# Kernel optimization log

Hardware: AMD Instinct MI355X
Metric: run time of the kernel (lower is better)

The kernel has to match this reference:

```python
import jax, jax.numpy as jnp
import numpy as np

L = 6      # num_coupling_layers
H = 256    # hidden_dims
B = 131072 # batch
D = 2      # sample_dims (fixed by masks)


def setup_inputs() -> dict:
    key = jax.random.key(0)
    ks = jax.random.split(key, 21)
    x = jax.random.uniform(ks[0], (B, D), jnp.float32, 1e-3, 1.0 - 1e-3)
    def w(k, shape):
        return jax.random.normal(k, shape, jnp.float32) * 0.05
    inp = {"x": x}
    shapes = {"W1": (L, D, H), "B1": (L, H), "W2": (L, H, H), "B2": (L, H),
              "W3": (L, H, H), "B3": (L, H), "W4": (L, H, H), "B4": (L, H),
              "W5": (L, H, D), "B5": (L, D)}
    i = 1
    for pref in ("s", "t"):
        for name, shp in shapes.items():
            inp[pref + name] = w(ks[i], shp)
            i += 1
    return inp


def _net(h, i, W1, B1, W2, B2, W3, B3, W4, B4, W5, B5, final_tanh):
    a = jax.nn.relu(h @ W1[i] + B1[i])
    a = jax.nn.relu(a @ W2[i] + B2[i])
    a = jax.nn.relu(a @ W3[i] + B3[i])
    a = jax.nn.relu(a @ W4[i] + B4[i])
    o = a @ W5[i] + B5[i]
    return jnp.tanh(o) if final_tanh else o


def reference(x, sW1, sB1, sW2, sB2, sW3, sB3, sW4, sB4, sW5, sB5,
              tW1, tB1, tW2, tB2, tW3, tB3, tW4, tB4, tW5, tB5):
    # masks alternate [0,1],[1,0]
    masks = jnp.asarray([[0.0, 1.0], [1.0, 0.0]] * (L // 2), jnp.float32)
    # logit transform
    x = -jnp.log(1.0 / x - 1.0)
    log_det_inv = jnp.zeros(x.shape[0], x.dtype)
    # training=True default -> direction = -1, gate = -1, reversed layer order
    for i in range(L - 1, -1, -1):
        m = masks[i]
        rm = 1.0 - m
        x_masked = x * m
        s = _net(x_masked, i, sW1, sB1, sW2, sB2, sW3, sB3, sW4, sB4, sW5, sB5, True) * rm
        t = _net(x_masked, i, tW1, tB1, tW2, tB2, tW3, tB3, tW4, tB4, tW5, tB5, False) * rm
        # rm*(x*exp(-s) - t*exp(-s)) + x_masked
        x = rm * ((x - t) * jnp.exp(-s)) + x_masked
        log_det_inv = log_det_inv - jnp.sum(s, axis=1)
    x = jax.nn.sigmoid(x)
    return x, log_det_inv
```

## Files before the change

kernel.cpp:

```cpp
#include <hip/hip_runtime.h>
#include <hip/hip_bf16.h>

#define LNUM 6
#define BATCH 131072

typedef __bf16 bf16x8 __attribute__((ext_vector_type(8)));
typedef float f32x16 __attribute__((ext_vector_type(16)));
typedef float f32x4  __attribute__((ext_vector_type(4)));

#define WFRAG_BYTES 131072ul
#define W1B1_OFF 4718592ul
#define BIAS_OFF 4743168ul
#define W5_OFF   4780032ul
#define NPT   2048
#define ZMIN  (-28.f)
#define ZH    (56.f / 2047.f)
#define ZINVH (2047.f / 56.f)
#define TABS_OFF 4793088ul
#define TABT_OFF 4842240ul
#define WS_NEEDED 4891392ul

struct PtrPack { const float* p[21]; };

__global__ void prep_all(PtrPack P, unsigned char* __restrict__ ws) {
    if (blockIdx.x < 288) {
#pragma unroll
        for (int r = 0; r < 4; ++r) {
            int t = blockIdx.x * 1024 + r * 256 + threadIdx.x;
            int blk = t >> 13;
            int e8  = t & 8191;
            int nh  = e8 >> 12;
            int kk  = (e8 >> 8) & 15;
            int nti = (e8 >> 6) & 3;
            int l   = e8 & 63;
            int nt = nh * 4 + nti;
            int n  = nt * 32 + (l & 31);
            int k0 = kk * 16 + (l >> 5) * 8;
            int net = blk / 18, rem = blk % 18;
            int i = rem / 3, g = rem % 3;
            const float* src = P.p[3 + g * 2 + net * 10] + i * 65536;
            bf16x8 v;
#pragma unroll
            for (int jj = 0; jj < 8; ++jj) v[jj] = (__bf16)src[(k0 + jj) * 256 + n];
            *(bf16x8*)(ws + (unsigned long)blk * WFRAG_BYTES + (unsigned)e8 * 16) = v;
        }
        return;
    }
#pragma unroll
    for (int r = 0; r < 8; ++r) {
        int t = (blockIdx.x - 288) * 2048 + r * 256 + threadIdx.x;
        if (t < 6144) {
            int idx = t >> 9, e = t & 511;
            int net = idx / 6, i = idx % 6;
            int j = (i & 1) ? 0 : 1;
            float v;
            if (e < 256) v = P.p[1 + net * 10][i * 512 + j * 256 + e];
            else         v = P.p[2 + net * 10][i * 256 + (e - 256)];
            ((float*)(ws + W1B1_OFF))[t] = v;
        } else if (t < 6144 + 9216) {
            int u = t - 6144;
            int idx = u >> 8, e = u & 255;
            int net = idx / 18, rem = idx % 18, i = rem / 3, g = rem % 3;
            ((float*)(ws + BIAS_OFF))[u] = P.p[4 + g * 2 + net * 10][i * 256 + e];
        } else if (t < 6144 + 9216 + 12 * 272) {
            int u = t - 6144 - 9216;
            int idx = u / 272, e = u % 272;
            int net = idx / 6, i = idx % 6;
            int ud = (i & 1) ? 1 : 0;
            float v = 0.f;
            if (e < 256)      v = P.p[9 + net * 10][i * 512 + e * 2 + ud];
            else if (e == 256) v = P.p[10 + net * 10][i * 2 + ud];
            ((float*)(ws + W5_OFF))[idx * 272 + e] = v;
        }
    }
}

#define L_A   0
#define L_ZG  65536
#define L_RED 66048
#define L_TOT 70144

__device__ __forceinline__ unsigned pk2(float a, float b) {
    unsigned short ua = __builtin_bit_cast(unsigned short, (__bf16)a);
    unsigned short ub = __builtin_bit_cast(unsigned short, (__bf16)b);
    return (unsigned)ua | ((unsigned)ub << 16);
}

__global__ __launch_bounds__(512, 1) void tab_eval(
        const unsigned char* __restrict__ ws, float* __restrict__ tabS,
        float* __restrict__ tabT) {
    __shared__ __align__(16) unsigned char lds[L_TOT];
    const int tid = threadIdx.x;
    const int wv = tid >> 6, lane = tid & 63;
    const int li = lane & 31, hi = lane >> 5;
    const int nn = blockIdx.x >> 4;
    const int tile = blockIdx.x & 15;
    float* zG  = (float*)(lds + L_ZG);
    float* red = (float*)(lds + L_RED);
    const float* w1b1_g = (const float*)(ws + W1B1_OFF);
    const float* bias_g = (const float*)(ws + BIAS_OFF);
    const float* w5_g   = (const float*)(ws + W5_OFF);

    const unsigned char* aaBase = lds + L_A + (unsigned)lane * 16;
    unsigned char* const stBase = lds + L_A + (unsigned)(li * 16 + hi * 8);

    if (tid < 128) zG[tid] = ZMIN + (float)(tile * 128 + tid) * ZH;
    __syncthreads();

    auto storeA = [&](const f32x16* a) {
#pragma unroll
        for (int rt = 0; rt < 4; ++rt)
#pragma unroll
            for (int q = 0; q < 4; ++q) {
                const f32x16& A = a[rt];
                unsigned lo = pk2(fmaxf(A[4 * q + 0], 0.f), fmaxf(A[4 * q + 1], 0.f));
                unsigned h2 = pk2(fmaxf(A[4 * q + 2], 0.f), fmaxf(A[4 * q + 3], 0.f));
                const unsigned off = (unsigned)((wv * 2 + (q >> 1)) * 4096
                                                + rt * 1024 + (q & 1) * 512);
                *(uint2*)(stBase + off) = make_uint2(lo, h2);
            }
    };

    {
        const float* w1 = w1b1_g + nn * 512;
        bf16x8 wf, af[4];
        const bf16x8 zr = {};
        if (hi == 0) {
            const int n = wv * 32 + li;
            const float W = w1[n], B = w1[256 + n];
            const __bf16 Wh = (__bf16)W;
            const __bf16 Wl = (__bf16)(W - (float)Wh);
            const __bf16 Bh = (__bf16)B;
            const __bf16 Bl = (__bf16)(B - (float)Bh);
            bf16x8 t = zr;
            t[0] = Wh; t[1] = Wl; t[2] = Wh; t[3] = Bh; t[4] = Bl;
            wf = t;
#pragma unroll
            for (int rt = 0; rt < 4; ++rt) {
                const float z = zG[rt * 32 + li];
                const __bf16 zh = (__bf16)z;
                const __bf16 zl = (__bf16)(z - (float)zh);
                bf16x8 t2 = zr;
                t2[0] = zh; t2[1] = zh; t2[2] = zl;
                t2[3] = (__bf16)1.f; t2[4] = (__bf16)1.f;
                af[rt] = t2;
            }
        } else {
            wf = zr;
            af[0] = zr; af[1] = zr; af[2] = zr; af[3] = zr;
        }
        f32x16 acc1[4];
#pragma unroll
        for (int u = 0; u < 4; ++u)
#pragma unroll
            for (int e = 0; e < 16; ++e) acc1[u][e] = 0.f;
#pragma unroll
        for (int rt = 0; rt < 4; ++rt)
            acc1[rt] = __builtin_amdgcn_mfma_f32_32x32x16_bf16(wf, af[rt], acc1[rt], 0, 0, 0);
        storeA(acc1);
    }
    __syncthreads();

#pragma unroll 1
    for (int g = 0; g < 3; ++g) {
        const int blk = nn * 3 + g;
        const unsigned char* wbase = ws + (unsigned long)blk * WFRAG_BYTES
                + (unsigned)(wv >> 2) * 65536 + (unsigned)(wv & 3) * 1024
                + (unsigned)lane * 16;
        const float* biasl = bias_g + blk * 256 + wv * 32;
        const float* w5 = w5_g + nn * 272;

        f32x16 acc[4];
#pragma unroll
        for (int q = 0; q < 4; ++q) {
            f32x4 bb = *(const f32x4*)(biasl + q * 8 + hi * 4);
#pragma unroll
            for (int rt = 0; rt < 4; ++rt) {
                acc[rt][4 * q + 0] = bb[0];
                acc[rt][4 * q + 1] = bb[1];
                acc[rt][4 * q + 2] = bb[2];
                acc[rt][4 * q + 3] = bb[3];
            }
        }
        bf16x8 wq[3];
#pragma unroll
        for (int p = 0; p < 3; ++p)
            wq[p] = *(const bf16x8*)(wbase + p * 4096);
        bf16x8 aa[2][4];
#pragma unroll
        for (int rt = 0; rt < 4; ++rt)
            aa[0][rt] = *(const bf16x8*)(aaBase + rt * 1024);
#pragma unroll
        for (int k = 0; k < 16; ++k) {
            const int cur = k & 1, nxt = cur ^ 1;
            if (k < 15) {
#pragma unroll
                for (int rt = 0; rt < 4; ++rt)
                    aa[nxt][rt] = *(const bf16x8*)(aaBase + (k + 1) * 4096 + rt * 1024);
            }
            __builtin_amdgcn_s_setprio(1);
#pragma unroll
            for (int rt = 0; rt < 4; ++rt)
                acc[rt] = __builtin_amdgcn_mfma_f32_32x32x16_bf16(wq[k % 3], aa[cur][rt], acc[rt], 0, 0, 0);
            __builtin_amdgcn_s_setprio(0);
            if (k < 13)
                wq[k % 3] = *(const bf16x8*)(wbase + (k + 3) * 4096);
        }
        __syncthreads();
        if (g < 2) {
            storeA(acc);
            __syncthreads();
        } else {
            float part[4] = {0.f, 0.f, 0.f, 0.f};
#pragma unroll
            for (int q = 0; q < 4; ++q) {
                f32x4 ww = *(const f32x4*)(w5 + wv * 32 + q * 8 + hi * 4);
#pragma unroll
                for (int rt = 0; rt < 4; ++rt)
#pragma unroll
                    for (int c = 0; c < 4; ++c)
                        part[rt] += fmaxf(acc[rt][4 * q + c], 0.f) * ww[c];
            }
#pragma unroll
            for (int rt = 0; rt < 4; ++rt) part[rt] += __shfl_xor(part[rt], 32);
            if (hi == 0) {
#pragma unroll
                for (int rt = 0; rt < 4; ++rt) red[wv * 128 + rt * 32 + li] = part[rt];
            }
            __syncthreads();
            if (tid < 128) {
                float o = w5[256];
#pragma unroll
                for (int w8 = 0; w8 < 8; ++w8) o += red[w8 * 128 + tid];
                const int pt = (nn % 6) * NPT + tile * 128 + tid;
                if (nn < 6) tabS[pt] = tanhf(o);
                else        tabT[pt] = o;
            }
        }
    }
}

__global__ __launch_bounds__(256) void apply_flow(
        const float* __restrict__ x, const float* __restrict__ tabS,
        const float* __restrict__ tabT, float* __restrict__ out) {
    const int r = blockIdx.x * 256 + threadIdx.x;
    const float4 xv = ((const float4*)x)[r];
    float zA0 = __logf(xv.x) - __logf(1.f - xv.x);
    float zB0 = __logf(xv.y) - __logf(1.f - xv.y);
    float zA1 = __logf(xv.z) - __logf(1.f - xv.z);
    float zB1 = __logf(xv.w) - __logf(1.f - xv.w);
    float ldt0 = 0.f, ldt1 = 0.f;
#pragma unroll
    for (int ii = 0; ii < LNUM; ++ii) {
        const int i = 5 - ii;
        const float* ts = tabS + i * NPT;
        const float* tt = tabT + i * NPT;
#pragma unroll
        for (int rr = 0; rr < 2; ++rr) {
            float& zA = rr ? zA1 : zA0;
            float& zB = rr ? zB1 : zB0;
            float& ldt = rr ? ldt1 : ldt0;
            const float zin = (i & 1) ? zA : zB;
            float u = (zin - ZMIN) * ZINVH;
            u = fminf(fmaxf(u, 0.f), (float)(NPT - 1) - 1e-3f);
            const int i0 = (int)u;
            const float fr = u - (float)i0;
            const float S = ts[i0] + (ts[i0 + 1] - ts[i0]) * fr;
            const float T = tt[i0] + (tt[i0 + 1] - tt[i0]) * fr;
            const float e = __expf(-S);
            if (i & 1) zB = (zB - T) * e;
            else       zA = (zA - T) * e;
            ldt -= S;
        }
    }
    ((float4*)out)[r] = make_float4(1.f / (1.f + __expf(-zA0)),
                                    1.f / (1.f + __expf(-zB0)),
                                    1.f / (1.f + __expf(-zA1)),
                                    1.f / (1.f + __expf(-zB1)));
    ((float2*)(out + 2 * BATCH))[r] = make_float2(ldt0, ldt1);
}

extern "C" void kernel_launch(void* const* d_in, const int* in_sizes, int n_in,
                              void* d_out, int out_size, void* d_ws, size_t ws_size,
                              hipStream_t stream) {
    if (ws_size < WS_NEEDED) return;
    PtrPack P;
    for (int k = 0; k < 21; ++k) P.p[k] = (const float*)d_in[k];
    unsigned char* ws = (unsigned char*)d_ws;
    float* tabS = (float*)(ws + TABS_OFF);
    float* tabT = (float*)(ws + TABT_OFF);
    prep_all<<<dim3(298), dim3(256), 0, stream>>>(P, ws);
    tab_eval<<<dim3(192), dim3(512), 0, stream>>>(ws, tabS, tabT);
    apply_flow<<<dim3(BATCH / 512), dim3(256), 0, stream>>>(
            (const float*)d_in[0], tabS, tabT, (float*)d_out);
}
```

Before: 33.02 us.

## Retile tab_eval waves as 2x4 grid and allow two blocks per CU

Each wave now computes 2 row tiles by 2 column tiles (64x64) instead of 4 row tiles by 1 column tile. This halves the LDS activation reads per wave while doubling the weight-fragment global loads. The reduction buffer shrinks so LDS drops below 68KB, and launch_bounds is raised to allow two blocks per CU for higher occupancy. The extra register pressure from two blocks may cause spills or throttling.

```diff
diff --git a/kernel.cpp b/kernel.cpp
--- a/kernel.cpp
+++ b/kernel.cpp
@@ -78,7 +78,7 @@
 #define L_A   0
 #define L_ZG  65536
 #define L_RED 66048
-#define L_TOT 70144
+#define L_TOT 68096
 
 __device__ __forceinline__ unsigned pk2(float a, float b) {
     unsigned short ua = __builtin_bit_cast(unsigned short, (__bf16)a);
@@ -86,13 +86,15 @@
     return (unsigned)ua | ((unsigned)ub << 16);
 }
 
-__global__ __launch_bounds__(512, 1) void tab_eval(
+__global__ __launch_bounds__(512, 2) void tab_eval(
         const unsigned char* __restrict__ ws, float* __restrict__ tabS,
         float* __restrict__ tabT) {
     __shared__ __align__(16) unsigned char lds[L_TOT];
     const int tid = threadIdx.x;
     const int wv = tid >> 6, lane = tid & 63;
     const int li = lane & 31, hi = lane >> 5;
+    const int rh = wv >> 2;
+    const int wc = wv & 3;
     const int nn = blockIdx.x >> 4;
     const int tile = blockIdx.x & 15;
     float* zG  = (float*)(lds + L_ZG);
@@ -109,45 +111,50 @@
 
     auto storeA = [&](const f32x16* a) {
 #pragma unroll
-        for (int rt = 0; rt < 4; ++rt)
-#pragma unroll
-            for (int q = 0; q < 4; ++q) {
-                const f32x16& A = a[rt];
-                unsigned lo = pk2(fmaxf(A[4 * q + 0], 0.f), fmaxf(A[4 * q + 1], 0.f));
-                unsigned h2 = pk2(fmaxf(A[4 * q + 2], 0.f), fmaxf(A[4 * q + 3], 0.f));
-                const unsigned off = (unsigned)((wv * 2 + (q >> 1)) * 4096
-                                                + rt * 1024 + (q & 1) * 512);
-                *(uint2*)(stBase + off) = make_uint2(lo, h2);
-            }
+        for (int rtl = 0; rtl < 2; ++rtl)
+#pragma unroll
+            for (int j2 = 0; j2 < 2; ++j2)
+#pragma unroll
+                for (int q = 0; q < 4; ++q) {
+                    const f32x16& A = a[rtl * 2 + j2];
+                    unsigned lo = pk2(fmaxf(A[4 * q + 0], 0.f), fmaxf(A[4 * q + 1], 0.f));
+                    unsigned h2 = pk2(fmaxf(A[4 * q + 2], 0.f), fmaxf(A[4 * q + 3], 0.f));
+                    const unsigned off = (unsigned)((wc * 4 + j2 * 2 + (q >> 1)) * 4096
+                                                    + (rh * 2 + rtl) * 1024 + (q & 1) * 512);
+                    *(uint2*)(stBase + off) = make_uint2(lo, h2);
+                }
     };
 
     {
         const float* w1 = w1b1_g + nn * 512;
-        bf16x8 wf, af[4];
+        bf16x8 wf[2], af[2];
         const bf16x8 zr = {};
         if (hi == 0) {
-            const int n = wv * 32 + li;
-            const float W = w1[n], B = w1[256 + n];
-            const __bf16 Wh = (__bf16)W;
-            const __bf16 Wl = (__bf16)(W - (float)Wh);
-            const __bf16 Bh = (__bf16)B;
-            const __bf16 Bl = (__bf16)(B - (float)Bh);
-            bf16x8 t = zr;
-            t[0] = Wh; t[1] = Wl; t[2] = Wh; t[3] = Bh; t[4] = Bl;
-            wf = t;
-#pragma unroll
-            for (int rt = 0; rt < 4; ++rt) {
-                const float z = zG[rt * 32 + li];
+#pragma unroll
+            for (int f = 0; f < 2; ++f) {
+                const int n = (wc * 2 + f) * 32 + li;
+                const float W = w1[n], B = w1[256 + n];
+                const __bf16 Wh = (__bf16)W;
+                const __bf16 Wl = (__bf16)(W - (float)Wh);
+                const __bf16 Bh = (__bf16)B;
+                const __bf16 Bl = (__bf16)(B - (float)Bh);
+                bf16x8 t = zr;
+                t[0] = Wh; t[1] = Wl; t[2] = Wh; t[3] = Bh; t[4] = Bl;
+                wf[f] = t;
+            }
+#pragma unroll
+            for (int rtl = 0; rtl < 2; ++rtl) {
+                const float z = zG[(rh * 2 + rtl) * 32 + li];
                 const __bf16 zh = (__bf16)z;
                 const __bf16 zl = (__bf16)(z - (float)zh);
                 bf16x8 t2 = zr;
                 t2[0] = zh; t2[1] = zh; t2[2] = zl;
                 t2[3] = (__bf16)1.f; t2[4] = (__bf16)1.f;
-                af[rt] = t2;
+                af[rtl] = t2;
             }
         } else {
-            wf = zr;
-            af[0] = zr; af[1] = zr; af[2] = zr; af[3] = zr;
+            wf[0] = zr; wf[1] = zr;
+            af[0] = zr; af[1] = zr;
         }
         f32x16 acc1[4];
 #pragma unroll
@@ -155,8 +162,10 @@
 #pragma unroll
             for (int e = 0; e < 16; ++e) acc1[u][e] = 0.f;
 #pragma unroll
-        for (int rt = 0; rt < 4; ++rt)
-            acc1[rt] = __builtin_amdgcn_mfma_f32_32x32x16_bf16(wf, af[rt], acc1[rt], 0, 0, 0);
+        for (int rtl = 0; rtl < 2; ++rtl) {
+            acc1[rtl * 2 + 0] = __builtin_amdgcn_mfma_f32_32x32x16_bf16(wf[0], af[rtl], acc1[rtl * 2 + 0], 0, 0, 0);
+            acc1[rtl * 2 + 1] = __builtin_amdgcn_mfma_f32_32x32x16_bf16(wf[1], af[rtl], acc1[rtl * 2 + 1], 0, 0, 0);
+        }
         storeA(acc1);
     }
     __syncthreads();
@@ -165,73 +174,87 @@
     for (int g = 0; g < 3; ++g) {
         const int blk = nn * 3 + g;
         const unsigned char* wbase = ws + (unsigned long)blk * WFRAG_BYTES
-                + (unsigned)(wv >> 2) * 65536 + (unsigned)(wv & 3) * 1024
+                + (unsigned)(wc >> 1) * 65536 + (unsigned)(wc & 1) * 2048
                 + (unsigned)lane * 16;
-        const float* biasl = bias_g + blk * 256 + wv * 32;
+        const float* biasl = bias_g + blk * 256 + wc * 64;
         const float* w5 = w5_g + nn * 272;
 
         f32x16 acc[4];
 #pragma unroll
-        for (int q = 0; q < 4; ++q) {
-            f32x4 bb = *(const f32x4*)(biasl + q * 8 + hi * 4);
-#pragma unroll
-            for (int rt = 0; rt < 4; ++rt) {
-                acc[rt][4 * q + 0] = bb[0];
-                acc[rt][4 * q + 1] = bb[1];
-                acc[rt][4 * q + 2] = bb[2];
-                acc[rt][4 * q + 3] = bb[3];
-            }
-        }
-        bf16x8 wq[3];
-#pragma unroll
-        for (int p = 0; p < 3; ++p)
-            wq[p] = *(const bf16x8*)(wbase + p * 4096);
-        bf16x8 aa[2][4];
-#pragma unroll
-        for (int rt = 0; rt < 4; ++rt)
-            aa[0][rt] = *(const bf16x8*)(aaBase + rt * 1024);
+        for (int j2 = 0; j2 < 2; ++j2)
+#pragma unroll
+            for (int q = 0; q < 4; ++q) {
+                f32x4 bb = *(const f32x4*)(biasl + j2 * 32 + q * 8 + hi * 4);
+#pragma unroll
+                for (int rtl = 0; rtl < 2; ++rtl) {
+                    acc[rtl * 2 + j2][4 * q + 0] = bb[0];
+                    acc[rtl * 2 + j2][4 * q + 1] = bb[1];
+                    acc[rtl * 2 + j2][4 * q + 2] = bb[2];
+                    acc[rtl * 2 + j2][4 * q + 3] = bb[3];
+                }
+            }
+        bf16x8 wq[3][2];
+#pragma unroll
+        for (int p = 0; p < 3; ++p) {
+            wq[p][0] = *(const bf16x8*)(wbase + p * 4096);
+            wq[p][1] = *(const bf16x8*)(wbase + p * 4096 + 1024);
+        }
+        bf16x8 aa[2][2];
+#pragma unroll
+        for (int rtl = 0; rtl < 2; ++rtl)
+            aa[0][rtl] = *(const bf16x8*)(aaBase + (rh * 2 + rtl) * 1024);
 #pragma unroll
         for (int k = 0; k < 16; ++k) {
             const int cur = k & 1, nxt = cur ^ 1;
             if (k < 15) {
 #pragma unroll
-                for (int rt = 0; rt < 4; ++rt)
-                    aa[nxt][rt] = *(const bf16x8*)(aaBase + (k + 1) * 4096 + rt * 1024);
+                for (int rtl = 0; rtl < 2; ++rtl)
+                    aa[nxt][rtl] = *(const bf16x8*)(aaBase + (k + 1) * 4096
+                                                    + (rh * 2 + rtl) * 1024);
             }
             __builtin_amdgcn_s_setprio(1);
 #pragma unroll
-            for (int rt = 0; rt < 4; ++rt)
-                acc[rt] = __builtin_amdgcn_mfma_f32_32x32x16_bf16(wq[k % 3], aa[cur][rt], acc[rt], 0, 0, 0);
+            for (int rtl = 0; rtl < 2; ++rtl) {
+                acc[rtl * 2 + 0] = __builtin_amdgcn_mfma_f32_32x32x16_bf16(wq[k % 3][0], aa[cur][rtl], acc[rtl * 2 + 0], 0, 0, 0);
+                acc[rtl * 2 + 1] = __builtin_amdgcn_mfma_f32_32x32x16_bf16(wq[k % 3][1], aa[cur][rtl], acc[rtl * 2 + 1], 0, 0, 0);
+            }
             __builtin_amdgcn_s_setprio(0);
-            if (k < 13)
-                wq[k % 3] = *(const bf16x8*)(wbase + (k + 3) * 4096);
+            if (k < 13) {
+                wq[k % 3][0] = *(const bf16x8*)(wbase + (k + 3) * 4096);
+                wq[k % 3][1] = *(const bf16x8*)(wbase + (k + 3) * 4096 + 1024);
+            }
         }
         __syncthreads();
         if (g < 2) {
             storeA(acc);
             __syncthreads();
         } else {
-            float part[4] = {0.f, 0.f, 0.f, 0.f};
-#pragma unroll
-            for (int q = 0; q < 4; ++q) {
-                f32x4 ww = *(const f32x4*)(w5 + wv * 32 + q * 8 + hi * 4);
-#pragma unroll
-                for (int rt = 0; rt < 4; ++rt)
-#pragma unroll
-                    for (int c = 0; c < 4; ++c)
-                        part[rt] += fmaxf(acc[rt][4 * q + c], 0.f) * ww[c];
-            }
-#pragma unroll
-            for (int rt = 0; rt < 4; ++rt) part[rt] += __shfl_xor(part[rt], 32);
+            float part[2] = {0.f, 0.f};
+#pragma unroll
+            for (int j2 = 0; j2 < 2; ++j2)
+#pragma unroll
+                for (int q = 0; q < 4; ++q) {
+                    f32x4 ww = *(const f32x4*)(w5 + wc * 64 + j2 * 32 + q * 8 + hi * 4);
+#pragma unroll
+                    for (int rtl = 0; rtl < 2; ++rtl)
+#pragma unroll
+                        for (int c = 0; c < 4; ++c)
+                            part[rtl] += fmaxf(acc[rtl * 2 + j2][4 * q + c], 0.f) * ww[c];
+                }
+#pragma unroll
+            for (int rtl = 0; rtl < 2; ++rtl) part[rtl] += __shfl_xor(part[rtl], 32);
             if (hi == 0) {
 #pragma unroll
-                for (int rt = 0; rt < 4; ++rt) red[wv * 128 + rt * 32 + li] = part[rt];
+                for (int rtl = 0; rtl < 2; ++rtl)
+                    red[wv * 64 + rtl * 32 + li] = part[rtl];
             }
             __syncthreads();
             if (tid < 128) {
+                const int rhh = tid >> 6, loc = tid & 63;
                 float o = w5[256];
 #pragma unroll
-                for (int w8 = 0; w8 < 8; ++w8) o += red[w8 * 128 + tid];
+                for (int w4 = 0; w4 < 4; ++w4)
+                    o += red[(rhh * 4 + w4) * 64 + loc];
                 const int pt = (nn % 6) * NPT + tile * 128 + tid;
                 if (nn < 6) tabS[pt] = tanhf(o);
                 else        tabT[pt] = o;
```

Measured after the change: 34.05 us. 3.1% more time.
